# Optimization experiments

Measured on AMD Instinct MI355X. Metric: run time of the kernel, lower is better.

Reference implementation:

```python
import jax, jax.numpy as jnp
import numpy as np

C = 256
RED = 8
CR = C // RED  # 32
B, H, W = 4, 64, 64
EPS = 1e-5


def setup_inputs() -> dict:
    key = jax.random.key(0)
    ks = jax.random.split(key, 12)
    s = 0.05
    return {
        "x": jax.random.normal(ks[0], (B, C, H, W), dtype=jnp.float32),
        "Wq": jax.random.normal(ks[1], (CR, C), dtype=jnp.float32) * s,
        "bq": jax.random.normal(ks[2], (CR,), dtype=jnp.float32) * s,
        "Wk": jax.random.normal(ks[3], (CR, C), dtype=jnp.float32) * s,
        "bk": jax.random.normal(ks[4], (CR,), dtype=jnp.float32) * s,
        "Wv": jax.random.normal(ks[5], (C, C), dtype=jnp.float32) * s,
        "bv": jax.random.normal(ks[6], (C,), dtype=jnp.float32) * s,
        "Wo": jax.random.normal(ks[7], (C, C), dtype=jnp.float32) * s,
        "bo": jax.random.normal(ks[8], (C,), dtype=jnp.float32) * s,
        "gamma": jnp.ones((C,), dtype=jnp.float32),
        "beta": jnp.zeros((C,), dtype=jnp.float32),
        "running_mean": jax.random.normal(ks[9], (C,), dtype=jnp.float32) * s,
        "running_var": jax.random.uniform(ks[10], (C,), dtype=jnp.float32, minval=0.5, maxval=1.5),
    }


def reference(x, Wq, bq, Wk, bk, Wv, bv, Wo, bo, gamma, beta, running_mean, running_var):
    b, c, h, w = x.shape
    n = h * w
    scale = c ** (-0.5)  # use_scale=True: in_channels**-0.5
    xf = x.reshape(b, c, n)  # [B, C, N]
    # 1x1 convs == per-pixel channel matmuls
    q = jnp.einsum('oc,bcn->bon', Wq, xf) + bq[None, :, None]   # [B, CR, N]
    k = jnp.einsum('oc,bcn->bon', Wk, xf) + bk[None, :, None]   # [B, CR, N]
    v = jnp.einsum('oc,bcn->bon', Wv, xf) + bv[None, :, None]   # [B, C, N]
    # attention[b, q_pos, k_pos], softmax over key positions (dim=2)
    attn = jnp.einsum('bcq,bck->bqk', q, k) * scale             # [B, N, N]
    attn = jax.nn.softmax(attn, axis=2)
    # out[b, c, q_pos] = sum_k v[b, c, k] * attn[b, q_pos, k]
    out = jnp.einsum('bck,bqk->bcq', v, attn)                   # [B, C, N]
    out = jnp.einsum('oc,bcn->bon', Wo, out) + bo[None, :, None]
    # BatchNorm2d (inference: running stats)
    inv = gamma / jnp.sqrt(running_var + EPS)
    out = out * inv[None, :, None] + (beta - running_mean * inv)[None, :, None]
    out = out.reshape(b, c, h, w)
    return jax.nn.relu(out + x)
```

## Files before the change

kernel.cpp:

```cpp
#include <hip/hip_runtime.h>
#include <hip/hip_bf16.h>

typedef unsigned short u16;
typedef unsigned int u32;

#define B_ 4
#define C_ 256
#define N_ 4096

constexpr float C1 = 0.09016844005556021f;

typedef float f32x16 __attribute__((ext_vector_type(16)));
typedef short bf16x8 __attribute__((ext_vector_type(8)));
typedef u32 u32x4 __attribute__((ext_vector_type(4)));
typedef int i32x2 __attribute__((ext_vector_type(2)));

__device__ __forceinline__ u16 bf16r(float f) {
    union { float f; u32 u; } a; a.f = f;
    u32 u = a.u;
    u += 0x7fffu + ((u >> 16) & 1u);
    return (u16)(u >> 16);
}

__device__ __forceinline__ float bf2f(u16 h) {
    union { u32 u; float f; } a; a.u = ((u32)h) << 16; return a.f;
}

__device__ __forceinline__ u32 pk2(float a, float b) {
    __hip_bfloat162 h = __float22bfloat162_rn(make_float2(a, b));
    union { __hip_bfloat162 h; u32 u; } c; c.h = h;
    return c.u;
}

__device__ __forceinline__ u32 cvtpk(float lo, float hi) {
    u32 r;
    asm("v_cvt_pk_bf16_f32 %0, %1, %2" : "=v"(r) : "v"(lo), "v"(hi));
    return r;
}

__device__ __forceinline__ void swap32(u32 &a, u32 &b) {
#if __has_builtin(__builtin_amdgcn_permlane32_swap)
    i32x2 r = __builtin_amdgcn_permlane32_swap((int)a, (int)b, false, false);
    a = (u32)r.x; b = (u32)r.y;
#else
    u32 as = __shfl_xor(a, 32), bs = __shfl_xor(b, 32);
    int hi = (threadIdx.x & 32) ? 1 : 0;
    u32 na = hi ? bs : a;
    u32 nb = hi ? b : as;
    a = na; b = nb;
#endif
}

__device__ __forceinline__ bf16x8 ld8(const u16* p) {
    return *reinterpret_cast<const bf16x8*>(p);
}

__device__ __forceinline__ void gld_lds16(const u16* g, u16* lbase, int lane) {
#if __has_builtin(__builtin_amdgcn_global_load_lds)
    __builtin_amdgcn_global_load_lds(
        (const __attribute__((address_space(1))) void*)g,
        (__attribute__((address_space(3))) void*)lbase, 16, 0, 0);
#else
    *reinterpret_cast<bf16x8*>(lbase + lane * 8) = ld8(g);
#endif
}

__device__ __forceinline__ int crow(int r, int hi) { return (r & 3) + 8 * (r >> 2) + 4 * hi; }

__global__ __launch_bounds__(256) void prep(
    const float* __restrict__ Wq, const float* __restrict__ Wk,
    const float* __restrict__ Wv, const float* __restrict__ Wo,
    const float* __restrict__ bo, const float* __restrict__ gamma,
    const float* __restrict__ beta, const float* __restrict__ rm, const float* __restrict__ rv,
    u16* __restrict__ wqk, u16* __restrict__ wv_b, u16* __restrict__ wo_b,
    float* __restrict__ scale, float* __restrict__ shift)
{
    int i = blockIdx.x * 256 + threadIdx.x;
    if (i < 16384) {
        float w = (i < 8192) ? Wq[i] * C1 : Wk[i - 8192];
        wqk[i] = bf16r(w);
    } else if (i < 81920) {
        wv_b[i - 16384] = bf16r(Wv[i - 16384]);
    } else if (i < 147456) {
        wo_b[i - 81920] = bf16r(Wo[i - 81920]);
    } else if (i < 147712) {
        int o = i - 147456;
        float inv = gamma[o] * rsqrtf(rv[o] + 1e-5f);
        scale[o] = inv;
        shift[o] = beta[o] + (bo[o] - rm[o]) * inv;
    }
}

__global__ __launch_bounds__(512) void projf(
    const float* __restrict__ x, const u16* __restrict__ wqk, const u16* __restrict__ wv,
    const float* __restrict__ bq, const float* __restrict__ bk, const float* __restrict__ bv,
    u16* __restrict__ qkt, u16* __restrict__ vout)
{
    __shared__ u16 xt[64 * 256];
    int tid = threadIdx.x;
    int lane = tid & 63, wid = tid >> 6;
    int r31 = lane & 31, hi = lane >> 5;
    int b = blockIdx.y, n0 = blockIdx.x * 64;
    const float* xb = x + (size_t)b * C_ * N_ + n0;
#pragma unroll
    for (int i = 0; i < 16; ++i) {
        int c2 = i * 8 + wid;
        int n = lane;
        float a0 = xb[(size_t)(2 * c2) * N_ + n];
        float a1 = xb[(size_t)(2 * c2 + 1) * N_ + n];
        int slot = (c2 >> 2) ^ (n & 31);
        *reinterpret_cast<u32*>(&xt[n * 256 + slot * 8 + (c2 & 3) * 2]) = pk2(a0, a1);
    }
    __syncthreads();
    for (int i = 0; i < 3; ++i) {
        int t = wid + i * 8;
        if (t < 20) {
            bool isqk = (t < 4);
            int nb = isqk ? (t >> 1) * 32 : ((t - 4) & 1) * 32;
            int gb = isqk ? (t & 1) * 32 : ((t - 4) >> 1) * 32;
            const u16* grow = (isqk ? wqk : wv) + (size_t)(gb + r31) * C_ + hi * 8;
            f32x16 acc;
#pragma unroll
            for (int r = 0; r < 16; ++r) acc[r] = 0.f;
#pragma unroll
            for (int ks = 0; ks < 16; ++ks) {
                int slot = (2 * ks + hi) ^ r31;
                bf16x8 lf = ld8(&xt[(nb + r31) * 256 + slot * 8]);
                bf16x8 gf = ld8(grow + ks * 16);
                if (isqk) acc = __builtin_amdgcn_mfma_f32_32x32x16_bf16(lf, gf, acc, 0, 0, 0);
                else      acc = __builtin_amdgcn_mfma_f32_32x32x16_bf16(gf, lf, acc, 0, 0, 0);
            }
            if (isqk) {
                int o = gb + r31;
                float bias = (o < 32) ? bq[o] * C1 : bk[o - 32];
                u16* qrow = qkt + ((size_t)b * N_ + n0 + nb) * 64 + o;
#pragma unroll
                for (int r = 0; r < 16; ++r)
                    qrow[(size_t)crow(r, hi) * 64] = bf16r(acc[r] + bias);
            } else {
                u16* vb = vout + (size_t)b * C_ * N_ + n0 + nb + r31;
#pragma unroll
                for (int r = 0; r < 16; ++r) {
                    int c = gb + crow(r, hi);
                    vb[(size_t)c * N_] = bf16r(acc[r] + bv[c]);
                }
            }
        }
    }
}

__global__ __launch_bounds__(256, 4) void attn(
    const u16* __restrict__ qkt, const u16* __restrict__ v,
    u16* __restrict__ opart, float* __restrict__ lpart, int kts)
{
    __shared__ u16 vt[256 * 64];
    __shared__ u16 ktt[64 * 32];
    int tid = threadIdx.x;
    int lane = tid & 63, wid = tid >> 6;
    int r31 = lane & 31, hi = lane >> 5;

    int nwg = 64 * 4 * gridDim.z;
    int wgl = blockIdx.x + 64 * (blockIdx.y + 4 * blockIdx.z);
    int cpx = nwg >> 3;
    int swzid = (wgl & 7) * cpx + (wgl >> 3);
    int bx = swzid & 63;
    int by = (swzid >> 6) & 3;
    int bz = swzid >> 8;

    int b = by, zs = bz;
    int q0 = bx * 64 + (wid >> 1) * 32;
    int cb = (wid & 1) * 128;
    const u16* qkb = qkt + (size_t)b * N_ * 64;
    const u16* vbase = v + (size_t)b * C_ * N_;

    int vc = tid >> 3;
    int vce = ((tid & 7) ^ (vc & 7)) << 3;
    int kr = tid >> 2;
    int kce = ((tid & 3) ^ (kr & 3)) << 3;
    u16* vlds = &vt[wid << 9];
    u16* klds = &ktt[wid << 9];

    int sw  = (r31 & 7) << 3;
    int ksw = (r31 & 3) << 3;

    bf16x8 qf0 = ld8(qkb + (size_t)(q0 + r31) * 64 + hi * 8);
    bf16x8 qf1 = ld8(qkb + (size_t)(q0 + r31) * 64 + 16 + hi * 8);

    f32x16 acc[4];
#pragma unroll
    for (int ct = 0; ct < 4; ++ct)
#pragma unroll
        for (int r = 0; r < 16; ++r) acc[ct][r] = 0.f;

    f32x16 z4;
#pragma unroll
    for (int r = 0; r < 16; ++r) z4[r] = 0.f;

    float l_run = 0.f;
    int ktBeg = zs * kts, ktEnd = (zs + 1) * kts;

    for (int kt = ktBeg; kt < ktEnd; ++kt) {
        int k0 = kt * 64;
        __syncthreads();
        gld_lds16(qkb + (size_t)(k0 + kr) * 64 + 32 + kce, klds, lane);
        {
            const u16* vsrc = vbase + (size_t)vc * N_ + k0 + vce;
#pragma unroll
            for (int i = 0; i < 8; ++i)
                gld_lds16(vsrc + (size_t)(32 * i) * N_, vlds + i * 2048, lane);
        }
        __syncthreads();

        float pst = 0.f;
#pragma unroll
        for (int ph = 0; ph < 2; ++ph) {
            int rowb = ph * 32;
            bf16x8 kf0 = ld8(&ktt[(rowb + r31) * 32 + ((hi * 8) ^ ksw)]);
            bf16x8 kf1 = ld8(&ktt[(rowb + r31) * 32 + ((16 + hi * 8) ^ ksw)]);
            f32x16 s = __builtin_amdgcn_mfma_f32_32x32x16_bf16(kf0, qf0, z4, 0, 0, 0);
            s = __builtin_amdgcn_mfma_f32_32x32x16_bf16(kf1, qf1, s, 0, 0, 0);
            float p[16];
#pragma unroll
            for (int r = 0; r < 16; ++r) { p[r] = __builtin_amdgcn_exp2f(s[r]); pst += p[r]; }
            bf16x8 pf[2];
#pragma unroll
            for (int c16 = 0; c16 < 2; ++c16) {
                u32 w0 = cvtpk(p[8 * c16 + 0], p[8 * c16 + 1]);
                u32 w1 = cvtpk(p[8 * c16 + 2], p[8 * c16 + 3]);
                u32 w2 = cvtpk(p[8 * c16 + 4], p[8 * c16 + 5]);
                u32 w3 = cvtpk(p[8 * c16 + 6], p[8 * c16 + 7]);
                swap32(w0, w2);
                swap32(w1, w3);
                union { bf16x8 f8; u32 u[4]; } fu;
                fu.u[0] = w0; fu.u[1] = w1; fu.u[2] = w2; fu.u[3] = w3;
                pf[c16] = fu.f8;
            }
            int kc0 = ph * 2;
#pragma unroll
            for (int ct = 0; ct < 4; ++ct) {
                int row = cb + ct * 32 + r31;
                bf16x8 vf0 = ld8(&vt[row * 64 + ((kc0 * 16 + hi * 8) ^ sw)]);
                bf16x8 vf1 = ld8(&vt[row * 64 + (((kc0 + 1) * 16 + hi * 8) ^ sw)]);
                acc[ct] = __builtin_amdgcn_mfma_f32_32x32x16_bf16(vf0, pf[0], acc[ct], 0, 0, 0);
                acc[ct] = __builtin_amdgcn_mfma_f32_32x32x16_bf16(vf1, pf[1], acc[ct], 0, 0, 0);
            }
        }
        pst += __shfl_xor(pst, 32);
        l_run += pst;
    }

    u16* dst = opart + ((size_t)(zs * B_ + b) * N_) * C_;
    if ((wid & 1) == 0 && hi == 0)
        lpart[((size_t)zs * B_ + b) * N_ + q0 + r31] = l_run;
    float (*tls)[32][33] = reinterpret_cast<float (*)[32][33]>(&vt[0]);
    int qg = lane >> 4, cd = lane & 15;
#pragma unroll
    for (int ct = 0; ct < 4; ++ct) {
        __syncthreads();
#pragma unroll
        for (int r = 0; r < 16; ++r)
            tls[wid][crow(r, hi)][r31] = acc[ct][r];
        __syncthreads();
#pragma unroll
        for (int it = 0; it < 8; ++it) {
            int qp = it * 4 + qg;
            u32 w = pk2(tls[wid][2 * cd][qp], tls[wid][2 * cd + 1][qp]);
            *reinterpret_cast<u32*>(dst + (size_t)(q0 + qp) * C_ + cb + ct * 32 + 2 * cd) = w;
        }
    }
}

__global__ __launch_bounds__(512) void outprojf(
    const u16* __restrict__ opart, const float* __restrict__ lpart,
    const u16* __restrict__ wo, const float* __restrict__ scl, const float* __restrict__ shf,
    const float* __restrict__ x, float* __restrict__ out, int S)
{
    __shared__ u16 ot[64 * 256];
    __shared__ float linv[64];
    int tid = threadIdx.x;
    int lane = tid & 63, wid = tid >> 6;
    int r31 = lane & 31, hi = lane >> 5;
    int b = blockIdx.y, n0 = blockIdx.x * 64;
    if (tid < 64) {
        float l = 0.f;
        for (int s = 0; s < S; ++s) l += lpart[((size_t)s * B_ + b) * N_ + n0 + tid];
        linv[tid] = 1.f / l;
    }
    __syncthreads();
#pragma unroll
    for (int i = 0; i < 4; ++i) {
        int chunk = i * 512 + tid;
        int n = chunk >> 5, c8 = chunk & 31;
        float a[8];
#pragma unroll
        for (int j = 0; j < 8; ++j) a[j] = 0.f;
        for (int s = 0; s < S; ++s) {
            bf16x8 o = ld8(opart + (((size_t)s * B_ + b) * N_ + n0 + n) * C_ + c8 * 8);
#pragma unroll
            for (int j = 0; j < 8; ++j) a[j] += bf2f((u16)o[j]);
        }
        float li = linv[n];
        u32x4 w;
#pragma unroll
        for (int j = 0; j < 4; ++j) w[j] = pk2(a[2 * j] * li, a[2 * j + 1] * li);
        int sws = c8 ^ (n & 31);
        *reinterpret_cast<u32x4*>(&ot[n * 256 + sws * 8]) = w;
    }
    __syncthreads();
    int obs = wid * 32;
    const u16* arow = wo + (size_t)(obs + r31) * C_ + hi * 8;
    f32x16 acc0, acc1;
#pragma unroll
    for (int r = 0; r < 16; ++r) { acc0[r] = 0.f; acc1[r] = 0.f; }
#pragma unroll
    for (int ks = 0; ks < 16; ++ks) {
        bf16x8 af = ld8(arow + ks * 16);
        int slot = (2 * ks + hi) ^ r31;
        bf16x8 b0 = ld8(&ot[r31 * 256 + slot * 8]);
        bf16x8 b1 = ld8(&ot[(32 + r31) * 256 + slot * 8]);
        acc0 = __builtin_amdgcn_mfma_f32_32x32x16_bf16(af, b0, acc0, 0, 0, 0);
        acc1 = __builtin_amdgcn_mfma_f32_32x32x16_bf16(af, b1, acc1, 0, 0, 0);
    }
    const float* xb = x + (size_t)b * C_ * N_;
    float* op = out + (size_t)b * C_ * N_;
#pragma unroll
    for (int r = 0; r < 16; ++r) {
        int o = obs + crow(r, hi);
        float sc = scl[o], sh = shf[o];
        size_t base = (size_t)o * N_ + n0;
        float v0 = acc0[r] * sc + sh + xb[base + r31];
        op[base + r31] = fmaxf(v0, 0.f);
        float v1 = acc1[r] * sc + sh + xb[base + 32 + r31];
        op[base + 32 + r31] = fmaxf(v1, 0.f);
    }
}

extern "C" void kernel_launch(void* const* d_in, const int* in_sizes, int n_in,
                              void* d_out, int out_size, void* d_ws, size_t ws_size,
                              hipStream_t stream) {
    const float* x     = (const float*)d_in[0];
    const float* Wq    = (const float*)d_in[1];
    const float* bq    = (const float*)d_in[2];
    const float* Wk    = (const float*)d_in[3];
    const float* bk    = (const float*)d_in[4];
    const float* Wv    = (const float*)d_in[5];
    const float* bv    = (const float*)d_in[6];
    const float* Wo    = (const float*)d_in[7];
    const float* bo    = (const float*)d_in[8];
    const float* gamma = (const float*)d_in[9];
    const float* beta  = (const float*)d_in[10];
    const float* rmean = (const float*)d_in[11];
    const float* rvar  = (const float*)d_in[12];
    float* out = (float*)d_out;

    char* ws = (char*)d_ws;
    u16* vbuf = (u16*)(ws);
    u16* qkt  = (u16*)(ws + (size_t)(8u << 20));
    char* wsm = ws + (size_t)(10u << 20);
    u16* wqk  = (u16*)(wsm);
    u16* wv_b = (u16*)(wsm + 32768);
    u16* wo_b = (u16*)(wsm + 32768 + 131072);
    float* scl = (float*)(wsm + 32768 + 262144);
    float* shf = scl + 256;
    float* lpart = (float*)(ws + (size_t)(11u << 20));
    u16* opart = (u16*)(ws + (size_t)(12u << 20));

    size_t need4 = (size_t)(12u << 20) + 4 * (size_t)(8u << 20);
    size_t need2 = (size_t)(12u << 20) + 2 * (size_t)(8u << 20);
    int S = (ws_size >= need4) ? 4 : (ws_size >= need2) ? 2 : 1;

    prep<<<dim3(578), dim3(256), 0, stream>>>(Wq, Wk, Wv, Wo, bo, gamma, beta, rmean, rvar,
                                              wqk, wv_b, wo_b, scl, shf);
    projf<<<dim3(64, 4), dim3(512), 0, stream>>>(x, wqk, wv_b, bq, bk, bv, qkt, vbuf);
    attn<<<dim3(64, 4, S), dim3(256), 0, stream>>>(qkt, vbuf, opart, lpart, 64 / S);
    outprojf<<<dim3(64, 4), dim3(512), 0, stream>>>(opart, lpart, wo_b, scl, shf, x, out, S);
}
```

Baseline: 91.50 us.

## Double-buffer K/V tiles in attention and widen blocks to 128 queries

After: 86.56 us. -5.4%, faster.

```diff
diff --git a/kernel.cpp b/kernel.cpp
--- a/kernel.cpp
+++ b/kernel.cpp
@@ -149,36 +149,34 @@
     }
 }
 
-__global__ __launch_bounds__(256, 4) void attn(
+__global__ __launch_bounds__(512, 4) void attn(
     const u16* __restrict__ qkt, const u16* __restrict__ v,
     u16* __restrict__ opart, float* __restrict__ lpart, int kts)
 {
-    __shared__ u16 vt[256 * 64];
-    __shared__ u16 ktt[64 * 32];
+    __shared__ u16 vt[2][256 * 64];
+    __shared__ u16 ktt[2][64 * 32];
     int tid = threadIdx.x;
     int lane = tid & 63, wid = tid >> 6;
     int r31 = lane & 31, hi = lane >> 5;
 
-    int nwg = 64 * 4 * gridDim.z;
-    int wgl = blockIdx.x + 64 * (blockIdx.y + 4 * blockIdx.z);
+    int nwg = 32 * 4 * gridDim.z;
+    int wgl = blockIdx.x + 32 * (blockIdx.y + 4 * blockIdx.z);
     int cpx = nwg >> 3;
     int swzid = (wgl & 7) * cpx + (wgl >> 3);
-    int bx = swzid & 63;
-    int by = (swzid >> 6) & 3;
-    int bz = swzid >> 8;
+    int bx = swzid & 31;
+    int by = (swzid >> 5) & 3;
+    int bz = swzid >> 7;
 
     int b = by, zs = bz;
-    int q0 = bx * 64 + (wid >> 1) * 32;
+    int q0 = bx * 128 + (wid >> 1) * 32;
     int cb = (wid & 1) * 128;
     const u16* qkb = qkt + (size_t)b * N_ * 64;
     const u16* vbase = v + (size_t)b * C_ * N_;
 
-    int vc = tid >> 3;
-    int vce = ((tid & 7) ^ (vc & 7)) << 3;
+    int vrb = tid >> 3;
+    int vce = ((tid & 7) ^ (vrb & 7)) << 3;
     int kr = tid >> 2;
     int kce = ((tid & 3) ^ (kr & 3)) << 3;
-    u16* vlds = &vt[wid << 9];
-    u16* klds = &ktt[wid << 9];
 
     int sw  = (r31 & 7) << 3;
     int ksw = (r31 & 3) << 3;
@@ -199,24 +197,29 @@
     float l_run = 0.f;
     int ktBeg = zs * kts, ktEnd = (zs + 1) * kts;
 
+    auto stage = [&](int buf, int kt) {
+        int k0 = kt * 64;
+        if (tid < 256)
+            gld_lds16(qkb + (size_t)(k0 + kr) * 64 + 32 + kce, &ktt[buf][(size_t)wid << 9], lane);
+        const u16* vsrc = vbase + (size_t)vrb * N_ + k0 + vce;
+#pragma unroll
+        for (int i = 0; i < 4; ++i)
+            gld_lds16(vsrc + (size_t)(64 * i) * N_, &vt[buf][(i * 512 + wid * 64) * 8], lane);
+    };
+
+    int cur = 0;
+    stage(cur, ktBeg);
+    __syncthreads();
+
     for (int kt = ktBeg; kt < ktEnd; ++kt) {
-        int k0 = kt * 64;
-        __syncthreads();
-        gld_lds16(qkb + (size_t)(k0 + kr) * 64 + 32 + kce, klds, lane);
-        {
-            const u16* vsrc = vbase + (size_t)vc * N_ + k0 + vce;
-#pragma unroll
-            for (int i = 0; i < 8; ++i)
-                gld_lds16(vsrc + (size_t)(32 * i) * N_, vlds + i * 2048, lane);
-        }
-        __syncthreads();
+        if (kt + 1 < ktEnd) stage(cur ^ 1, kt + 1);
 
         float pst = 0.f;
 #pragma unroll
         for (int ph = 0; ph < 2; ++ph) {
             int rowb = ph * 32;
-            bf16x8 kf0 = ld8(&ktt[(rowb + r31) * 32 + ((hi * 8) ^ ksw)]);
-            bf16x8 kf1 = ld8(&ktt[(rowb + r31) * 32 + ((16 + hi * 8) ^ ksw)]);
+            bf16x8 kf0 = ld8(&ktt[cur][(rowb + r31) * 32 + ((hi * 8) ^ ksw)]);
+            bf16x8 kf1 = ld8(&ktt[cur][(rowb + r31) * 32 + ((16 + hi * 8) ^ ksw)]);
             f32x16 s = __builtin_amdgcn_mfma_f32_32x32x16_bf16(kf0, qf0, z4, 0, 0, 0);
             s = __builtin_amdgcn_mfma_f32_32x32x16_bf16(kf1, qf1, s, 0, 0, 0);
             float p[16];
@@ -239,20 +242,23 @@
 #pragma unroll
             for (int ct = 0; ct < 4; ++ct) {
                 int row = cb + ct * 32 + r31;
-                bf16x8 vf0 = ld8(&vt[row * 64 + ((kc0 * 16 + hi * 8) ^ sw)]);
-                bf16x8 vf1 = ld8(&vt[row * 64 + (((kc0 + 1) * 16 + hi * 8) ^ sw)]);
+                bf16x8 vf0 = ld8(&vt[cur][row * 64 + ((kc0 * 16 + hi * 8) ^ sw)]);
+                bf16x8 vf1 = ld8(&vt[cur][row * 64 + (((kc0 + 1) * 16 + hi * 8) ^ sw)]);
                 acc[ct] = __builtin_amdgcn_mfma_f32_32x32x16_bf16(vf0, pf[0], acc[ct], 0, 0, 0);
                 acc[ct] = __builtin_amdgcn_mfma_f32_32x32x16_bf16(vf1, pf[1], acc[ct], 0, 0, 0);
             }
         }
         pst += __shfl_xor(pst, 32);
         l_run += pst;
+
+        __syncthreads();
+        cur ^= 1;
     }
 
     u16* dst = opart + ((size_t)(zs * B_ + b) * N_) * C_;
     if ((wid & 1) == 0 && hi == 0)
         lpart[((size_t)zs * B_ + b) * N_ + q0 + r31] = l_run;
-    float (*tls)[32][33] = reinterpret_cast<float (*)[32][33]>(&vt[0]);
+    float (*tls)[32][33] = reinterpret_cast<float (*)[32][33]>(&vt[0][0]);
     int qg = lane >> 4, cd = lane & 15;
 #pragma unroll
     for (int ct = 0; ct < 4; ++ct) {
@@ -372,6 +378,6 @@
     prep<<<dim3(578), dim3(256), 0, stream>>>(Wq, Wk, Wv, Wo, bo, gamma, beta, rmean, rvar,
                                               wqk, wv_b, wo_b, scl, shf);
     projf<<<dim3(64, 4), dim3(512), 0, stream>>>(x, wqk, wv_b, bq, bk, bv, qkt, vbuf);
-    attn<<<dim3(64, 4, S), dim3(256), 0, stream>>>(qkt, vbuf, opart, lpart, 64 / S);
+    attn<<<dim3(32, 4, S), dim3(512), 0, stream>>>(qkt, vbuf, opart, lpart, 64 / S);
     outprojf<<<dim3(64, 4), dim3(512), 0, stream>>>(opart, lpart, wo_b, scl, shf, x, out, S);
 }
```
